# Kernel tuning notes

Hardware: AMD Instinct MI355X
Metric: run time of the kernel (lower is better)

## Reference

```python
import jax, jax.numpy as jnp
import numpy as np


def setup_inputs() -> dict:
    key = jax.random.key(0)
    k1, k2 = jax.random.split(key)
    N, K, D = 400000, 50, 256
    locF = jax.random.normal(k1, (N, 1, D), dtype=jnp.float32)
    Ck = jax.random.normal(k2, (1, K, D), dtype=jnp.float32)
    return {"locF": locF, "Ck": Ck}


def reference(locF, Ck):
    # locF: [N, 1, D], Ck: [1, k, D]
    x = locF[:, 0, :]            # [N, D]
    c = Ck[0]                    # [k, D]
    k, D = c.shape
    # mean squared distance: ((x - c)**2).mean(-1) expanded to avoid [N,k,D] intermediate
    x2 = jnp.sum(x * x, axis=1, keepdims=True)        # [N, 1]
    c2 = jnp.sum(c * c, axis=1)                       # [k]
    d2 = (x2 - 2.0 * (x @ c.T) + c2) / D              # [N, k]
    index = jnp.argmin(d2, axis=1)                    # [N]
    # single-pass scatter-add of sums and counts keyed by argmin
    sums = jax.ops.segment_sum(x, index, num_segments=k)   # [k, D]
    counts = jnp.zeros((k,), dtype=jnp.int32).at[index].add(1)
    Ck1 = sums[None]            # [1, k, D]  (matches torch.cat along dim=1 of [1,1,D] chunks)
    nItems = counts[None]       # [1, k]
    return Ck1, nItems
```

## Files before the change

kernel.cpp:

```cpp
#include <hip/hip_runtime.h>


typedef _Float16 f16x8 __attribute__((ext_vector_type(8)));
typedef float    f32x4 __attribute__((ext_vector_type(4)));
typedef float    f32x16 __attribute__((ext_vector_type(16)));
typedef unsigned int u32x4 __attribute__((ext_vector_type(4)));

constexpr int K = 50, KP = 64, D = 256, KD = K * D;
constexpr int BLK = 1024, GRID = 512, CH = 32;
constexpr int SSTH = 72;
constexpr int PST  = 40;

__global__ __launch_bounds__(BLK)
void k_fused(const float* __restrict__ x, const float* __restrict__ cc,
             float* __restrict__ partial, float* __restrict__ out,
             int N, int useAtomic) {
    __shared__ _Float16       sC[K * D];
    __shared__ unsigned short sxh[2][CH * D];
    __shared__ alignas(16) _Float16 sS0[32 * SSTH];
    __shared__ alignas(16) _Float16 sS1[32 * SSTH];
    __shared__ alignas(16) _Float16 sPT[2][64 * PST];
    __shared__ float          sc2[KP];
    __shared__ int            scnt[K];

    const int tid = threadIdx.x;
    for (int i = tid; i < K * D; i += BLK) sC[i] = (_Float16)0.f;
    for (int i = tid; i < 2 * 64 * PST; i += BLK) sPT[0][i] = (_Float16)0.f;
    if (tid < K) scnt[tid] = 0;
    __syncthreads();
    for (int i = tid; i < KD; i += BLK) {
        int r = i >> 8, col = i & 255, ch = col >> 3, wd = col & 7;
        sC[r * D + (((ch ^ (r & 7)) << 3) | wd)] = (_Float16)cc[i];
    }
    if (tid < KP) {
        float s = 0.f;
        if (tid < K) for (int q = 0; q < D; ++q) { float v = cc[tid * D + q]; s += v * v; }
        sc2[tid] = s;
    }
    __syncthreads();

    const int lane = tid & 63, ci = lane & 15, g = lane >> 4, w = tid >> 6;
    const int kh   = (w >= 14) ? 1 : 0;
    const int wA   = w & 1;
    const int ra   = lane & 31;
    const int dl   = lane >> 5;
    const int rakey = (ra & 7) ^ (((ra >> 3) & 1) << 2);
    const int cl32 = wA * 32 + (lane & 31);
    const int clkey = (lane & 31) & 7;
    const _Float16* cbp = &sC[(cl32 < K ? cl32 : K - 1) * D];
    const int bcol = w * 16 + ci, bc3 = bcol >> 3, bce = bcol & 7;

    const int nCh = N / CH;
    const int cpb = nCh / gridDim.x, rem = nCh % gridDim.x;
    const int bid = blockIdx.x;
    const int lo  = bid * cpb + (bid < rem ? bid : rem);
    const int cnt = cpb + (bid < rem ? 1 : 0);

    const float INF = 3.4e38f;
    const float c2A = (cl32 < K) ? sc2[cl32] : INF;

    const int srow = 2 * w + (lane >> 5);
    const int scol = (lane & 31);
    const int skey = (srow & 7) ^ (((srow >> 3) & 1) << 2);
    f32x4 rA = {0,0,0,0}, rB = {0,0,0,0};
#define ISSUE(t_) { const float* b_ = x + (size_t)(t_) * (CH * D) + srow * D + 8 * scol; \
    rA = *(const f32x4*)(b_); rB = *(const f32x4*)(b_ + 4); }
#define WSLOT(s_) { \
    f16x8 h_ = {(_Float16)rA[0], (_Float16)rA[1], (_Float16)rA[2], (_Float16)rA[3], \
                (_Float16)rB[0], (_Float16)rB[1], (_Float16)rB[2], (_Float16)rB[3]}; \
    *(f16x8*)(&sxh[s_][srow * D + ((scol ^ skey) << 3)]) = h_; }

    f32x4 bacc0 = {0,0,0,0}, bacc1 = {0,0,0,0}, bacc2 = {0,0,0,0}, bacc3 = {0,0,0,0};

    if (cnt > 0) { ISSUE(lo) WSLOT(0) if (cnt > 1) ISSUE(lo + 1) }
    __syncthreads();

    for (int i = 0; i <= cnt; ++i) {
        if (i >= 1) {
            const unsigned short* xbh = &sxh[(i - 1) & 1][0];
            const _Float16* pt = &sPT[(i - 1) & 1][0];
            unsigned short v0, v1, v2, v3, v4, v5, v6, v7;
#define RDH(j) { const int p_ = 8 * g + (j); const int key_ = (j) ^ ((g & 1) << 2); \
            v##j = xbh[p_ * D + ((bc3 ^ key_) << 3) + bce]; }
            RDH(0) RDH(1) RDH(2) RDH(3) RDH(4) RDH(5) RDH(6) RDH(7)
#undef RDH
            unsigned int w0 = (unsigned int)v0 | ((unsigned int)v1 << 16);
            unsigned int w1 = (unsigned int)v2 | ((unsigned int)v3 << 16);
            unsigned int w2 = (unsigned int)v4 | ((unsigned int)v5 << 16);
            unsigned int w3 = (unsigned int)v6 | ((unsigned int)v7 << 16);
            u32x4 W = {w0, w1, w2, w3};
            f16x8 bfr = __builtin_bit_cast(f16x8, W);
            __builtin_amdgcn_s_setprio(1);
#define BMT(M, ACC) { \
            f16x8 a = *(const f16x8*)(pt + ((M) * 16 + ci) * PST + 8 * g); \
            ACC = __builtin_amdgcn_mfma_f32_16x16x32_f16(a, bfr, ACC, 0, 0, 0); }
            BMT(0, bacc0) BMT(1, bacc1) BMT(2, bacc2) BMT(3, bacc3)
#undef BMT
            __builtin_amdgcn_s_setprio(0);
        }

        if (w >= 12 && i < cnt) {
            const unsigned short* xb = &sxh[i & 1][0];
            f32x16 acc = {0,0,0,0,0,0,0,0,0,0,0,0,0,0,0,0};
            __builtin_amdgcn_s_setprio(1);
#define A_KS(s) { \
            const int c_ = (kh * 8 + (s)) * 2 + dl; \
            f16x8 a = *(const f16x8*)(&xb[ra * D + ((c_ ^ rakey) << 3)]); \
            f16x8 b = *(const f16x8*)(cbp + ((c_ ^ clkey) << 3)); \
            acc = __builtin_amdgcn_mfma_f32_32x32x16_f16(a, b, acc, 0, 0, 0); }
            A_KS(0) A_KS(1) A_KS(2) A_KS(3) A_KS(4) A_KS(5) A_KS(6) A_KS(7)
#undef A_KS
            __builtin_amdgcn_s_setprio(0);
            if (kh == 0) {
#define DUMP(r) { const int row_ = ((r) & 3) + 8 * ((r) >> 2) + 4 * dl; \
                sS0[row_ * SSTH + cl32] = (_Float16)(c2A - 2.f * acc[r]); }
                DUMP(0) DUMP(1) DUMP(2) DUMP(3) DUMP(4) DUMP(5) DUMP(6) DUMP(7)
                DUMP(8) DUMP(9) DUMP(10) DUMP(11) DUMP(12) DUMP(13) DUMP(14) DUMP(15)
#undef DUMP
            } else {
#define DUMP(r) { const int row_ = ((r) & 3) + 8 * ((r) >> 2) + 4 * dl; \
                sS1[row_ * SSTH + cl32] = (_Float16)(-2.f * acc[r]); }
                DUMP(0) DUMP(1) DUMP(2) DUMP(3) DUMP(4) DUMP(5) DUMP(6) DUMP(7)
                DUMP(8) DUMP(9) DUMP(10) DUMP(11) DUMP(12) DUMP(13) DUMP(14) DUMP(15)
#undef DUMP
            }
        }

        __syncthreads();

        if (i + 1 < cnt) {
            WSLOT((i + 1) & 1)
            if (i + 2 < cnt) ISSUE(lo + i + 2)
        }

        if (w < 8 && i + 1 < cnt) {
            const int z = w * 64 + lane;
            if (z < (64 * PST * 2) / 16) {
                f16x8 zz = {(_Float16)0.f,(_Float16)0.f,(_Float16)0.f,(_Float16)0.f,
                            (_Float16)0.f,(_Float16)0.f,(_Float16)0.f,(_Float16)0.f};
                *(f16x8*)(&sPT[(i + 1) & 1][z * 8]) = zz;
            }
        }

        if (w >= 8 && w < 12 && i < cnt) {
            const int p_ = (w - 8) * 8 + (lane >> 3);
            const int q  = lane & 7;
            const _Float16* s0p = &sS0[p_ * SSTH + 8 * q];
            const _Float16* s1p = &sS1[p_ * SSTH + 8 * q];
            f16x8 h0 = *(const f16x8*)(s0p);
            f16x8 h1 = *(const f16x8*)(s1p);
            float bm = (float)h0[0] + (float)h1[0]; int bb = 8 * q;
#define CMP(E) { float s_ = (float)h0[E] + (float)h1[E]; int c_ = 8 * q + (E); \
            if (s_ < bm) { bm = s_; bb = c_; } }
            CMP(1) CMP(2) CMP(3) CMP(4) CMP(5) CMP(6) CMP(7)
#undef CMP
            { float pm = __shfl_xor(bm, 1, 64); int pb = __shfl_xor(bb, 1, 64);
              if (pm < bm || (pm == bm && pb < bb)) { bm = pm; bb = pb; } }
            { float pm = __shfl_xor(bm, 2, 64); int pb = __shfl_xor(bb, 2, 64);
              if (pm < bm || (pm == bm && pb < bb)) { bm = pm; bb = pb; } }
            { float pm = __shfl_xor(bm, 4, 64); int pb = __shfl_xor(bb, 4, 64);
              if (pm < bm || (pm == bm && pb < bb)) { bm = pm; bb = pb; } }
            if (q == 0) {
                sPT[i & 1][bb * PST + p_] = (_Float16)1.f;
                atomicAdd(&scnt[bb], 1);
            }
        }
        __syncthreads();
    }

    if (useAtomic) {
#define WBK(M, ACC) { \
        { int cl_ = (M)*16 + 4*g + 0; if (cl_ < K) atomicAdd(&out[cl_ * D + bcol], ACC[0]); } \
        { int cl_ = (M)*16 + 4*g + 1; if (cl_ < K) atomicAdd(&out[cl_ * D + bcol], ACC[1]); } \
        { int cl_ = (M)*16 + 4*g + 2; if (cl_ < K) atomicAdd(&out[cl_ * D + bcol], ACC[2]); } \
        { int cl_ = (M)*16 + 4*g + 3; if (cl_ < K) atomicAdd(&out[cl_ * D + bcol], ACC[3]); } }
        WBK(0, bacc0) WBK(1, bacc1) WBK(2, bacc2) WBK(3, bacc3)
#undef WBK
    } else {
        float* pb = partial + (size_t)bid * KD;
#define WBK(M, ACC) { \
        { int cl_ = (M)*16 + 4*g + 0; if (cl_ < K) pb[cl_ * D + bcol] = ACC[0]; } \
        { int cl_ = (M)*16 + 4*g + 1; if (cl_ < K) pb[cl_ * D + bcol] = ACC[1]; } \
        { int cl_ = (M)*16 + 4*g + 2; if (cl_ < K) pb[cl_ * D + bcol] = ACC[2]; } \
        { int cl_ = (M)*16 + 4*g + 3; if (cl_ < K) pb[cl_ * D + bcol] = ACC[3]; } }
        WBK(0, bacc0) WBK(1, bacc1) WBK(2, bacc2) WBK(3, bacc3)
#undef WBK
    }
    __syncthreads();
    for (int k = tid; k < K; k += BLK) atomicAdd(&out[KD + k], (float)scnt[k]);
}

__global__ __launch_bounds__(256)
void k_reduce(const float* __restrict__ partial, float* __restrict__ out, int G) {
    const int j  = blockIdx.x * 256 + threadIdx.x;
    const int bs = G / 8;
    const int b0 = blockIdx.y * bs;
    float s = 0.f;
    for (int b = b0; b < b0 + bs; ++b) s += partial[(size_t)b * KD + j];
    atomicAdd(&out[j], s);
}

extern "C" void kernel_launch(void* const* d_in, const int* in_sizes, int n_in,
                              void* d_out, int out_size, void* d_ws, size_t ws_size,
                              hipStream_t stream) {
    const float* x = (const float*)d_in[0];
    const float* c = (const float*)d_in[1];
    float* out = (float*)d_out;
    const int N = in_sizes[0] / D;

    float* partial = (float*)d_ws;
    const size_t need = (size_t)GRID * KD * sizeof(float);
    const int useAtomic = (ws_size < need) ? 1 : 0;

    hipMemsetAsync(d_out, 0, (size_t)out_size * sizeof(float), stream);
    k_fused<<<GRID, BLK, 0, stream>>>(x, c, partial, out, N, useAtomic);
    if (!useAtomic) {
        k_reduce<<<dim3(KD / 256, 8), 256, 0, stream>>>(partial, out, GRID);
    }
}
```

Measured before the change: 134.2 us.

## Compute full-K distance GEMM per wave and fuse argmin in registers

The distance GEMM is restructured: instead of four waves each computing half the reduction and dumping fp16 partial scores to shared memory for a separate argmin stage, two waves each run the full 16-step K reduction with the centroid/x operands swapped. Each wave then reduces its accumulators in fp32 registers to a per-point min and index, and a single half-wave picks between the two cluster halves. This drops the fp16 score buffers, the extra shared-memory round trip and the four argmin waves, and it avoids fp16 rounding of scores. In exchange, each GEMM wave does twice the MFMA chain serially, so per-iteration latency on the critical path may grow.

Result: slower. 154.6 us (+15.2%).

```diff
diff --git a/kernel.cpp b/kernel.cpp
--- a/kernel.cpp
+++ b/kernel.cpp
@@ -8,7 +8,6 @@
 
 constexpr int K = 50, KP = 64, D = 256, KD = K * D;
 constexpr int BLK = 1024, GRID = 512, CH = 32;
-constexpr int SSTH = 72;
 constexpr int PST  = 40;
 
 __global__ __launch_bounds__(BLK)
@@ -17,10 +16,10 @@
              int N, int useAtomic) {
     __shared__ _Float16       sC[K * D];
     __shared__ unsigned short sxh[2][CH * D];
-    __shared__ alignas(16) _Float16 sS0[32 * SSTH];
-    __shared__ alignas(16) _Float16 sS1[32 * SSTH];
     __shared__ alignas(16) _Float16 sPT[2][64 * PST];
     __shared__ float          sc2[KP];
+    __shared__ float          sAM[2][CH];
+    __shared__ int            sAI[2][CH];
     __shared__ int            scnt[K];
 
     const int tid = threadIdx.x;
@@ -33,20 +32,22 @@
         sC[r * D + (((ch ^ (r & 7)) << 3) | wd)] = (_Float16)cc[i];
     }
     if (tid < KP) {
-        float s = 0.f;
-        if (tid < K) for (int q = 0; q < D; ++q) { float v = cc[tid * D + q]; s += v * v; }
+        float s = 3.4e38f;
+        if (tid < K) {
+            s = 0.f;
+            for (int q = 0; q < D; ++q) { float v = cc[tid * D + q]; s += v * v; }
+        }
         sc2[tid] = s;
     }
     __syncthreads();
 
     const int lane = tid & 63, ci = lane & 15, g = lane >> 4, w = tid >> 6;
-    const int kh   = (w >= 14) ? 1 : 0;
     const int wA   = w & 1;
-    const int ra   = lane & 31;
+    const int pl   = lane & 31;
     const int dl   = lane >> 5;
-    const int rakey = (ra & 7) ^ (((ra >> 3) & 1) << 2);
-    const int cl32 = wA * 32 + (lane & 31);
-    const int clkey = (lane & 31) & 7;
+    const int xkey = (pl & 7) ^ (((pl >> 3) & 1) << 2);
+    const int cl32 = wA * 32 + pl;
+    const int clkey = pl & 7;
     const _Float16* cbp = &sC[(cl32 < K ? cl32 : K - 1) * D];
     const int bcol = w * 16 + ci, bc3 = bcol >> 3, bce = bcol & 7;
 
@@ -55,9 +56,6 @@
     const int bid = blockIdx.x;
     const int lo  = bid * cpb + (bid < rem ? bid : rem);
     const int cnt = cpb + (bid < rem ? 1 : 0);
-
-    const float INF = 3.4e38f;
-    const float c2A = (cl32 < K) ? sc2[cl32] : INF;
 
     const int srow = 2 * w + (lane >> 5);
     const int scol = (lane & 31);
@@ -99,31 +97,35 @@
             __builtin_amdgcn_s_setprio(0);
         }
 
-        if (w >= 12 && i < cnt) {
+        if (w >= 14 && i < cnt) {
             const unsigned short* xb = &sxh[i & 1][0];
             f32x16 acc = {0,0,0,0,0,0,0,0,0,0,0,0,0,0,0,0};
             __builtin_amdgcn_s_setprio(1);
-#define A_KS(s) { \
-            const int c_ = (kh * 8 + (s)) * 2 + dl; \
-            f16x8 a = *(const f16x8*)(&xb[ra * D + ((c_ ^ rakey) << 3)]); \
-            f16x8 b = *(const f16x8*)(cbp + ((c_ ^ clkey) << 3)); \
+#define A_KS(ks) { \
+            const int c_ = (ks) * 2 + dl; \
+            f16x8 a = *(const f16x8*)(cbp + ((c_ ^ clkey) << 3));           \
+            f16x8 b = *(const f16x8*)(&xb[pl * D + ((c_ ^ xkey) << 3)]);    \
             acc = __builtin_amdgcn_mfma_f32_32x32x16_f16(a, b, acc, 0, 0, 0); }
             A_KS(0) A_KS(1) A_KS(2) A_KS(3) A_KS(4) A_KS(5) A_KS(6) A_KS(7)
+            A_KS(8) A_KS(9) A_KS(10) A_KS(11) A_KS(12) A_KS(13) A_KS(14) A_KS(15)
 #undef A_KS
             __builtin_amdgcn_s_setprio(0);
-            if (kh == 0) {
-#define DUMP(r) { const int row_ = ((r) & 3) + 8 * ((r) >> 2) + 4 * dl; \
-                sS0[row_ * SSTH + cl32] = (_Float16)(c2A - 2.f * acc[r]); }
-                DUMP(0) DUMP(1) DUMP(2) DUMP(3) DUMP(4) DUMP(5) DUMP(6) DUMP(7)
-                DUMP(8) DUMP(9) DUMP(10) DUMP(11) DUMP(12) DUMP(13) DUMP(14) DUMP(15)
-#undef DUMP
-            } else {
-#define DUMP(r) { const int row_ = ((r) & 3) + 8 * ((r) >> 2) + 4 * dl; \
-                sS1[row_ * SSTH + cl32] = (_Float16)(-2.f * acc[r]); }
-                DUMP(0) DUMP(1) DUMP(2) DUMP(3) DUMP(4) DUMP(5) DUMP(6) DUMP(7)
-                DUMP(8) DUMP(9) DUMP(10) DUMP(11) DUMP(12) DUMP(13) DUMP(14) DUMP(15)
-#undef DUMP
-            }
+            float bm = 3.4e38f; int bb = 0;
+#define AQ(q) { \
+            f32x4 c2q = *(const f32x4*)(&sc2[32 * wA + 4 * dl + 8 * (q)]); \
+            { float s_ = c2q[0] - 2.f * acc[4*(q)+0]; int c_ = 32*wA + 4*dl + 8*(q) + 0; \
+              if (s_ < bm || (s_ == bm && c_ < bb)) { bm = s_; bb = c_; } } \
+            { float s_ = c2q[1] - 2.f * acc[4*(q)+1]; int c_ = 32*wA + 4*dl + 8*(q) + 1; \
+              if (s_ < bm || (s_ == bm && c_ < bb)) { bm = s_; bb = c_; } } \
+            { float s_ = c2q[2] - 2.f * acc[4*(q)+2]; int c_ = 32*wA + 4*dl + 8*(q) + 2; \
+              if (s_ < bm || (s_ == bm && c_ < bb)) { bm = s_; bb = c_; } } \
+            { float s_ = c2q[3] - 2.f * acc[4*(q)+3]; int c_ = 32*wA + 4*dl + 8*(q) + 3; \
+              if (s_ < bm || (s_ == bm && c_ < bb)) { bm = s_; bb = c_; } } }
+            AQ(0) AQ(1) AQ(2) AQ(3)
+#undef AQ
+            { float pm = __shfl_xor(bm, 32, 64); int pb = __shfl_xor(bb, 32, 64);
+              if (pm < bm || (pm == bm && pb < bb)) { bm = pm; bb = pb; } }
+            if (lane < 32) { sAM[wA][pl] = bm; sAI[wA][pl] = bb; }
         }
 
         __syncthreads();
@@ -142,28 +144,12 @@
             }
         }
 
-        if (w >= 8 && w < 12 && i < cnt) {
-            const int p_ = (w - 8) * 8 + (lane >> 3);
-            const int q  = lane & 7;
-            const _Float16* s0p = &sS0[p_ * SSTH + 8 * q];
-            const _Float16* s1p = &sS1[p_ * SSTH + 8 * q];
-            f16x8 h0 = *(const f16x8*)(s0p);
-            f16x8 h1 = *(const f16x8*)(s1p);
-            float bm = (float)h0[0] + (float)h1[0]; int bb = 8 * q;
-#define CMP(E) { float s_ = (float)h0[E] + (float)h1[E]; int c_ = 8 * q + (E); \
-            if (s_ < bm) { bm = s_; bb = c_; } }
-            CMP(1) CMP(2) CMP(3) CMP(4) CMP(5) CMP(6) CMP(7)
-#undef CMP
-            { float pm = __shfl_xor(bm, 1, 64); int pb = __shfl_xor(bb, 1, 64);
-              if (pm < bm || (pm == bm && pb < bb)) { bm = pm; bb = pb; } }
-            { float pm = __shfl_xor(bm, 2, 64); int pb = __shfl_xor(bb, 2, 64);
-              if (pm < bm || (pm == bm && pb < bb)) { bm = pm; bb = pb; } }
-            { float pm = __shfl_xor(bm, 4, 64); int pb = __shfl_xor(bb, 4, 64);
-              if (pm < bm || (pm == bm && pb < bb)) { bm = pm; bb = pb; } }
-            if (q == 0) {
-                sPT[i & 1][bb * PST + p_] = (_Float16)1.f;
-                atomicAdd(&scnt[bb], 1);
-            }
+        if (w == 8 && lane < 32 && i < cnt) {
+            float m0 = sAM[0][lane], m1 = sAM[1][lane];
+            int   b0 = sAI[0][lane], b1 = sAI[1][lane];
+            const int best = (m1 < m0 || (m1 == m0 && b1 < b0)) ? b1 : b0;
+            sPT[i & 1][best * PST + lane] = (_Float16)1.f;
+            atomicAdd(&scnt[best], 1);
         }
         __syncthreads();
     }
```

## Rebalance distance MFMA across 8 waves, triple-buffer assignment tiles, drop memset

Applied to the files above, without the earlier changes.

Distance computation moves from 4 waves doing 32x32x16 MFMAs with split-K halves onto 8 waves doing 16x16x32 MFMAs over the full K, which removes the second score buffer and the add step in the argmin. The argmin stage now runs on waves 0-7 at 4 elements per lane and reduces over 16 lanes. The one-hot assignment tile is triple-buffered and sized to 50 rows. Counts are written into the per-block partial, and the reduce kernel does one non-atomic pass per output element, so the memset is skipped when the workspace is large enough. The reduce now has far fewer threads, each looping over all 512 partials, which may cost more than the atomics it removes.

New measurement: 232.7 us. 73.5% more time.

```diff
diff --git a/kernel.cpp b/kernel.cpp
--- a/kernel.cpp
+++ b/kernel.cpp
@@ -2,14 +2,16 @@
 
 
 typedef _Float16 f16x8 __attribute__((ext_vector_type(8)));
+typedef _Float16 f16x4 __attribute__((ext_vector_type(4)));
 typedef float    f32x4 __attribute__((ext_vector_type(4)));
-typedef float    f32x16 __attribute__((ext_vector_type(16)));
 typedef unsigned int u32x4 __attribute__((ext_vector_type(4)));
 
 constexpr int K = 50, KP = 64, D = 256, KD = K * D;
+constexpr int OUT_N = KD + K;
 constexpr int BLK = 1024, GRID = 512, CH = 32;
 constexpr int SSTH = 72;
 constexpr int PST  = 40;
+constexpr int PTR  = 50;
 
 __global__ __launch_bounds__(BLK)
 void k_fused(const float* __restrict__ x, const float* __restrict__ cc,
@@ -17,15 +19,14 @@
              int N, int useAtomic) {
     __shared__ _Float16       sC[K * D];
     __shared__ unsigned short sxh[2][CH * D];
-    __shared__ alignas(16) _Float16 sS0[32 * SSTH];
-    __shared__ alignas(16) _Float16 sS1[32 * SSTH];
-    __shared__ alignas(16) _Float16 sPT[2][64 * PST];
+    __shared__ alignas(16) _Float16 sS[32 * SSTH];
+    __shared__ alignas(16) _Float16 sPT[3][PTR * PST];
     __shared__ float          sc2[KP];
     __shared__ int            scnt[K];
 
     const int tid = threadIdx.x;
     for (int i = tid; i < K * D; i += BLK) sC[i] = (_Float16)0.f;
-    for (int i = tid; i < 2 * 64 * PST; i += BLK) sPT[0][i] = (_Float16)0.f;
+    for (int i = tid; i < 3 * PTR * PST; i += BLK) sPT[0][i] = (_Float16)0.f;
     if (tid < K) scnt[tid] = 0;
     __syncthreads();
     for (int i = tid; i < KD; i += BLK) {
@@ -40,24 +41,26 @@
     __syncthreads();
 
     const int lane = tid & 63, ci = lane & 15, g = lane >> 4, w = tid >> 6;
-    const int kh   = (w >= 14) ? 1 : 0;
-    const int wA   = w & 1;
-    const int ra   = lane & 31;
-    const int dl   = lane >> 5;
-    const int rakey = (ra & 7) ^ (((ra >> 3) & 1) << 2);
-    const int cl32 = wA * 32 + (lane & 31);
-    const int clkey = (lane & 31) & 7;
-    const _Float16* cbp = &sC[(cl32 < K ? cl32 : K - 1) * D];
+    const int pt   = (w - 8) & 1;
+    const int ncl  = ((w - 8) >> 1) & 3;
+    const int arow = pt * 16 + ci;
+    const int akey = (ci & 7) ^ (((ci >> 3) & 1) << 2);
+    const int acl  = ncl * 16 + ci;
+    const int ackey = ci & 7;
+    const _Float16* cbp = &sC[(acl < K ? acl : K - 1) * D];
+    const float INF = 3.4e38f;
+    const float c2v = (acl < K) ? sc2[acl] : INF;
     const int bcol = w * 16 + ci, bc3 = bcol >> 3, bce = bcol & 7;
+    const int pr0 = ci;
+    const int pr1 = 16 + ci;
+    const int pr2 = 32 + ci;
+    const int pr3 = (48 + ci < K) ? (48 + ci) : (K - 1);
 
     const int nCh = N / CH;
     const int cpb = nCh / gridDim.x, rem = nCh % gridDim.x;
     const int bid = blockIdx.x;
     const int lo  = bid * cpb + (bid < rem ? bid : rem);
     const int cnt = cpb + (bid < rem ? 1 : 0);
-
-    const float INF = 3.4e38f;
-    const float c2A = (cl32 < K) ? sc2[cl32] : INF;
 
     const int srow = 2 * w + (lane >> 5);
     const int scol = (lane & 31);
@@ -78,7 +81,7 @@
     for (int i = 0; i <= cnt; ++i) {
         if (i >= 1) {
             const unsigned short* xbh = &sxh[(i - 1) & 1][0];
-            const _Float16* pt = &sPT[(i - 1) & 1][0];
+            const _Float16* ptb = &sPT[(i - 1) % 3][0];
             unsigned short v0, v1, v2, v3, v4, v5, v6, v7;
 #define RDH(j) { const int p_ = 8 * g + (j); const int key_ = (j) ^ ((g & 1) << 2); \
             v##j = xbh[p_ * D + ((bc3 ^ key_) << 3) + bce]; }
@@ -91,39 +94,29 @@
             u32x4 W = {w0, w1, w2, w3};
             f16x8 bfr = __builtin_bit_cast(f16x8, W);
             __builtin_amdgcn_s_setprio(1);
-#define BMT(M, ACC) { \
-            f16x8 a = *(const f16x8*)(pt + ((M) * 16 + ci) * PST + 8 * g); \
+#define BMT(PR, ACC) { \
+            f16x8 a = *(const f16x8*)(ptb + (PR) * PST + 8 * g); \
             ACC = __builtin_amdgcn_mfma_f32_16x16x32_f16(a, bfr, ACC, 0, 0, 0); }
-            BMT(0, bacc0) BMT(1, bacc1) BMT(2, bacc2) BMT(3, bacc3)
+            BMT(pr0, bacc0) BMT(pr1, bacc1) BMT(pr2, bacc2) BMT(pr3, bacc3)
 #undef BMT
             __builtin_amdgcn_s_setprio(0);
         }
 
-        if (w >= 12 && i < cnt) {
+        if (w >= 8 && i < cnt) {
             const unsigned short* xb = &sxh[i & 1][0];
-            f32x16 acc = {0,0,0,0,0,0,0,0,0,0,0,0,0,0,0,0};
+            f32x4 acc = {0.f, 0.f, 0.f, 0.f};
             __builtin_amdgcn_s_setprio(1);
-#define A_KS(s) { \
-            const int c_ = (kh * 8 + (s)) * 2 + dl; \
-            f16x8 a = *(const f16x8*)(&xb[ra * D + ((c_ ^ rakey) << 3)]); \
-            f16x8 b = *(const f16x8*)(cbp + ((c_ ^ clkey) << 3)); \
-            acc = __builtin_amdgcn_mfma_f32_32x32x16_f16(a, b, acc, 0, 0, 0); }
+#define A_KS(ks) { \
+            f16x8 a = *(const f16x8*)(&xb[arow * D + ((((ks) * 4 + g) ^ akey) << 3)]); \
+            f16x8 b = *(const f16x8*)(cbp + ((((ks) * 4 + g) ^ ackey) << 3)); \
+            acc = __builtin_amdgcn_mfma_f32_16x16x32_f16(a, b, acc, 0, 0, 0); }
             A_KS(0) A_KS(1) A_KS(2) A_KS(3) A_KS(4) A_KS(5) A_KS(6) A_KS(7)
 #undef A_KS
             __builtin_amdgcn_s_setprio(0);
-            if (kh == 0) {
-#define DUMP(r) { const int row_ = ((r) & 3) + 8 * ((r) >> 2) + 4 * dl; \
-                sS0[row_ * SSTH + cl32] = (_Float16)(c2A - 2.f * acc[r]); }
-                DUMP(0) DUMP(1) DUMP(2) DUMP(3) DUMP(4) DUMP(5) DUMP(6) DUMP(7)
-                DUMP(8) DUMP(9) DUMP(10) DUMP(11) DUMP(12) DUMP(13) DUMP(14) DUMP(15)
-#undef DUMP
-            } else {
-#define DUMP(r) { const int row_ = ((r) & 3) + 8 * ((r) >> 2) + 4 * dl; \
-                sS1[row_ * SSTH + cl32] = (_Float16)(-2.f * acc[r]); }
-                DUMP(0) DUMP(1) DUMP(2) DUMP(3) DUMP(4) DUMP(5) DUMP(6) DUMP(7)
-                DUMP(8) DUMP(9) DUMP(10) DUMP(11) DUMP(12) DUMP(13) DUMP(14) DUMP(15)
-#undef DUMP
-            }
+            sS[(pt * 16 + 4 * g + 0) * SSTH + acl] = (_Float16)(c2v - 2.f * acc[0]);
+            sS[(pt * 16 + 4 * g + 1) * SSTH + acl] = (_Float16)(c2v - 2.f * acc[1]);
+            sS[(pt * 16 + 4 * g + 2) * SSTH + acl] = (_Float16)(c2v - 2.f * acc[2]);
+            sS[(pt * 16 + 4 * g + 3) * SSTH + acl] = (_Float16)(c2v - 2.f * acc[3]);
         }
 
         __syncthreads();
@@ -133,36 +126,35 @@
             if (i + 2 < cnt) ISSUE(lo + i + 2)
         }
 
-        if (w < 8 && i + 1 < cnt) {
-            const int z = w * 64 + lane;
-            if (z < (64 * PST * 2) / 16) {
-                f16x8 zz = {(_Float16)0.f,(_Float16)0.f,(_Float16)0.f,(_Float16)0.f,
-                            (_Float16)0.f,(_Float16)0.f,(_Float16)0.f,(_Float16)0.f};
-                *(f16x8*)(&sPT[(i + 1) & 1][z * 8]) = zz;
+        if (w < 8) {
+            if (i + 1 < cnt) {
+                const int z = w * 64 + lane;
+                if (z < (PTR * PST) / 8) {
+                    f16x8 zz = {(_Float16)0.f,(_Float16)0.f,(_Float16)0.f,(_Float16)0.f,
+                                (_Float16)0.f,(_Float16)0.f,(_Float16)0.f,(_Float16)0.f};
+                    *(f16x8*)(&sPT[(i + 1) % 3][z * 8]) = zz;
+                }
             }
-        }
-
-        if (w >= 8 && w < 12 && i < cnt) {
-            const int p_ = (w - 8) * 8 + (lane >> 3);
-            const int q  = lane & 7;
-            const _Float16* s0p = &sS0[p_ * SSTH + 8 * q];
-            const _Float16* s1p = &sS1[p_ * SSTH + 8 * q];
-            f16x8 h0 = *(const f16x8*)(s0p);
-            f16x8 h1 = *(const f16x8*)(s1p);
-            float bm = (float)h0[0] + (float)h1[0]; int bb = 8 * q;
-#define CMP(E) { float s_ = (float)h0[E] + (float)h1[E]; int c_ = 8 * q + (E); \
-            if (s_ < bm) { bm = s_; bb = c_; } }
-            CMP(1) CMP(2) CMP(3) CMP(4) CMP(5) CMP(6) CMP(7)
-#undef CMP
-            { float pm = __shfl_xor(bm, 1, 64); int pb = __shfl_xor(bb, 1, 64);
-              if (pm < bm || (pm == bm && pb < bb)) { bm = pm; bb = pb; } }
-            { float pm = __shfl_xor(bm, 2, 64); int pb = __shfl_xor(bb, 2, 64);
-              if (pm < bm || (pm == bm && pb < bb)) { bm = pm; bb = pb; } }
-            { float pm = __shfl_xor(bm, 4, 64); int pb = __shfl_xor(bb, 4, 64);
-              if (pm < bm || (pm == bm && pb < bb)) { bm = pm; bb = pb; } }
-            if (q == 0) {
-                sPT[i & 1][bb * PST + p_] = (_Float16)1.f;
-                atomicAdd(&scnt[bb], 1);
+            if (i < cnt) {
+                const int p_ = w * 4 + (lane >> 4);
+                const int cg = lane & 15;
+                f16x4 hv = *(const f16x4*)(&sS[p_ * SSTH + 4 * cg]);
+                float bm = (float)hv[0]; int bb = 4 * cg;
+                { float s_ = (float)hv[1]; if (s_ < bm) { bm = s_; bb = 4 * cg + 1; } }
+                { float s_ = (float)hv[2]; if (s_ < bm) { bm = s_; bb = 4 * cg + 2; } }
+                { float s_ = (float)hv[3]; if (s_ < bm) { bm = s_; bb = 4 * cg + 3; } }
+                { float pm = __shfl_xor(bm, 1, 64); int pb = __shfl_xor(bb, 1, 64);
+                  if (pm < bm || (pm == bm && pb < bb)) { bm = pm; bb = pb; } }
+                { float pm = __shfl_xor(bm, 2, 64); int pb = __shfl_xor(bb, 2, 64);
+                  if (pm < bm || (pm == bm && pb < bb)) { bm = pm; bb = pb; } }
+                { float pm = __shfl_xor(bm, 4, 64); int pb = __shfl_xor(bb, 4, 64);
+                  if (pm < bm || (pm == bm && pb < bb)) { bm = pm; bb = pb; } }
+                { float pm = __shfl_xor(bm, 8, 64); int pb = __shfl_xor(bb, 8, 64);
+                  if (pm < bm || (pm == bm && pb < bb)) { bm = pm; bb = pb; } }
+                if (cg == 0) {
+                    sPT[i % 3][bb * PST + p_] = (_Float16)1.f;
+                    atomicAdd(&scnt[bb], 1);
+                }
             }
         }
         __syncthreads();
@@ -176,8 +168,10 @@
         { int cl_ = (M)*16 + 4*g + 3; if (cl_ < K) atomicAdd(&out[cl_ * D + bcol], ACC[3]); } }
         WBK(0, bacc0) WBK(1, bacc1) WBK(2, bacc2) WBK(3, bacc3)
 #undef WBK
+        __syncthreads();
+        for (int k = tid; k < K; k += BLK) atomicAdd(&out[KD + k], (float)scnt[k]);
     } else {
-        float* pb = partial + (size_t)bid * KD;
+        float* pb = partial + (size_t)bid * OUT_N;
 #define WBK(M, ACC) { \
         { int cl_ = (M)*16 + 4*g + 0; if (cl_ < K) pb[cl_ * D + bcol] = ACC[0]; } \
         { int cl_ = (M)*16 + 4*g + 1; if (cl_ < K) pb[cl_ * D + bcol] = ACC[1]; } \
@@ -185,19 +179,18 @@
         { int cl_ = (M)*16 + 4*g + 3; if (cl_ < K) pb[cl_ * D + bcol] = ACC[3]; } }
         WBK(0, bacc0) WBK(1, bacc1) WBK(2, bacc2) WBK(3, bacc3)
 #undef WBK
-    }
-    __syncthreads();
-    for (int k = tid; k < K; k += BLK) atomicAdd(&out[KD + k], (float)scnt[k]);
+        __syncthreads();
+        for (int k = tid; k < K; k += BLK) pb[KD + k] = (float)scnt[k];
+    }
 }
 
 __global__ __launch_bounds__(256)
 void k_reduce(const float* __restrict__ partial, float* __restrict__ out, int G) {
-    const int j  = blockIdx.x * 256 + threadIdx.x;
-    const int bs = G / 8;
-    const int b0 = blockIdx.y * bs;
+    const int j = blockIdx.x * 256 + threadIdx.x;
+    if (j >= OUT_N) return;
     float s = 0.f;
-    for (int b = b0; b < b0 + bs; ++b) s += partial[(size_t)b * KD + j];
-    atomicAdd(&out[j], s);
+    for (int b = 0; b < G; ++b) s += partial[(size_t)b * OUT_N + j];
+    out[j] = s;
 }
 
 extern "C" void kernel_launch(void* const* d_in, const int* in_sizes, int n_in,
@@ -209,12 +202,14 @@
     const int N = in_sizes[0] / D;
 
     float* partial = (float*)d_ws;
-    const size_t need = (size_t)GRID * KD * sizeof(float);
+    const size_t need = (size_t)GRID * OUT_N * sizeof(float);
     const int useAtomic = (ws_size < need) ? 1 : 0;
 
-    hipMemsetAsync(d_out, 0, (size_t)out_size * sizeof(float), stream);
+    if (useAtomic) {
+        hipMemsetAsync(d_out, 0, (size_t)out_size * sizeof(float), stream);
+    }
     k_fused<<<GRID, BLK, 0, stream>>>(x, c, partial, out, N, useAtomic);
     if (!useAtomic) {
-        k_reduce<<<dim3(KD / 256, 8), 256, 0, stream>>>(partial, out, GRID);
+        k_reduce<<<(OUT_N + 255) / 256, 256, 0, stream>>>(partial, out, GRID);
     }
 }
```
